# Kernel tuning notes

Hardware: AMD Instinct MI355X
Metric: run time of the kernel (lower is better)

Reference implementation:

```python
import jax, jax.numpy as jnp
import numpy as np

N = 50000       # nodes
E = 800000      # edges
F_IN = 128      # num_features
DIM = 64        # dim
D0 = 4 * DIM    # layer-0 width = 256
G = 256         # num graphs
EPS_BN = 1e-5


def _init_linear(key, fan_in, fan_out, bias=True):
    k1, k2 = jax.random.split(key)
    W = jax.random.normal(k1, (fan_in, fan_out), jnp.float32) * (1.0 / np.sqrt(fan_in))
    if bias:
        b = jax.random.normal(k2, (fan_out,), jnp.float32) * 0.01
        return W, b
    return W


def setup_inputs() -> dict:
    key = jax.random.key(0)
    ks = jax.random.split(key, 16)
    x = jax.random.normal(ks[0], (N, F_IN), jnp.float32)
    edge_index = jax.random.randint(ks[1], (2, E), 0, N, jnp.int32)
    edge_attr = jax.random.normal(ks[2], (E, 1), jnp.float32)
    batch = jnp.sort(jax.random.randint(ks[3], (N,), 0, G, jnp.int32))
    # conv0: in F_IN -> out D0, heads=1, edge_dim=1
    Wq0, bq0 = _init_linear(ks[4], F_IN, D0)
    Wk0, bk0 = _init_linear(ks[5], F_IN, D0)
    Wv0, bv0 = _init_linear(ks[6], F_IN, D0)
    We0 = _init_linear(ks[7], 1, D0, bias=False)   # lin_edge has no bias in PyG
    Ws0, bs0 = _init_linear(ks[8], F_IN, D0)       # lin_skip (root weight)
    # conv1: in D0 -> out DIM
    Wq1, bq1 = _init_linear(ks[9], D0, DIM)
    Wk1, bk1 = _init_linear(ks[10], D0, DIM)
    Wv1, bv1 = _init_linear(ks[11], D0, DIM)
    We1 = _init_linear(ks[12], 1, DIM, bias=False)
    Ws1, bs1 = _init_linear(ks[13], D0, DIM)
    # BatchNorm affine params
    gamma0 = jnp.ones((D0,), jnp.float32)
    beta0 = jnp.zeros((D0,), jnp.float32)
    gamma1 = jnp.ones((DIM,), jnp.float32)
    beta1 = jnp.zeros((DIM,), jnp.float32)
    return dict(x=x, edge_index=edge_index, edge_attr=edge_attr, batch=batch,
                Wq0=Wq0, bq0=bq0, Wk0=Wk0, bk0=bk0, Wv0=Wv0, bv0=bv0, We0=We0, Ws0=Ws0, bs0=bs0,
                gamma0=gamma0, beta0=beta0,
                Wq1=Wq1, bq1=bq1, Wk1=Wk1, bk1=bk1, Wv1=Wv1, bv1=bv1, We1=We1, Ws1=Ws1, bs1=bs1,
                gamma1=gamma1, beta1=beta1)


def _transformer_conv(x, edge_index, edge_attr, Wq, bq, Wk, bk, Wv, bv, We, Ws, bs):
    # PyG TransformerConv, heads=1, concat=True, root_weight=True, beta=False
    src, dst = edge_index[0], edge_index[1]
    n, d = x.shape[0], Wq.shape[1]
    q = x @ Wq + bq            # [N, d]
    k = x @ Wk + bk
    v = x @ Wv + bv
    e = edge_attr @ We          # [E, d]
    ke = k[src] + e             # key_j + edge embedding
    logits = jnp.sum(q[dst] * ke, axis=-1) / jnp.sqrt(jnp.asarray(d, jnp.float32))  # [E]
    # scatter-softmax over incoming edges of each dst node
    m = jax.ops.segment_max(logits, dst, num_segments=n)
    p = jnp.exp(logits - m[dst])
    s = jax.ops.segment_sum(p, dst, num_segments=n)
    alpha = p / (s[dst] + 1e-16)
    msg = (v[src] + e) * alpha[:, None]              # [E, d]
    out = jax.ops.segment_sum(msg, dst, num_segments=n)
    return out + x @ Ws + bs                          # root/skip connection


def _batch_norm(x, gamma, beta):
    mu = jnp.mean(x, axis=0)
    var = jnp.mean(jnp.square(x - mu), axis=0)  # biased var (torch training mode)
    return gamma * (x - mu) * jax.lax.rsqrt(var + EPS_BN) + beta


def _global_mean_pool(x, batch, num_graphs):
    s = jax.ops.segment_sum(x, batch, num_segments=num_graphs)
    c = jax.ops.segment_sum(jnp.ones((x.shape[0],), x.dtype), batch, num_segments=num_graphs)
    return s / jnp.maximum(c, 1.0)[:, None]


def reference(x, edge_index, edge_attr, batch,
              Wq0, bq0, Wk0, bk0, Wv0, bv0, We0, Ws0, bs0, gamma0, beta0,
              Wq1, bq1, Wk1, bk1, Wv1, bv1, We1, Ws1, bs1, gamma1, beta1):
    h0 = _batch_norm(_transformer_conv(x, edge_index, edge_attr,
                                       Wq0, bq0, Wk0, bk0, Wv0, bv0, We0, Ws0, bs0),
                     gamma0, beta0)                  # [N, D0]
    h1 = _batch_norm(_transformer_conv(h0, edge_index, edge_attr,
                                       Wq1, bq1, Wk1, bk1, Wv1, bv1, We1, Ws1, bs1),
                     gamma1, beta1)                  # [N, DIM]
    xpool = jnp.concatenate([_global_mean_pool(h0, batch, G),
                             _global_mean_pool(h1, batch, G)], axis=1)  # [G, D0+DIM]
    xs = jnp.concatenate([h0, h1], axis=1)                               # [N, D0+DIM]
    return (xpool, xs)
```

## Files before the change

kernel.cpp:

```cpp
#include <hip/hip_runtime.h>

constexpr int NN = 50000;
constexpr int NE = 800000;
constexpr int F_IN = 128;
constexpr int D0 = 256;
constexpr int D1 = 64;
constexpr int NG = 256;
constexpr float EPS_BN = 1e-5f;

typedef __attribute__((ext_vector_type(8))) short bf16x8;
typedef __attribute__((ext_vector_type(4))) float f32x4;
typedef __attribute__((ext_vector_type(8))) ushort u16x8;
typedef __attribute__((ext_vector_type(4))) ushort u16x4;

__device__ inline ushort f2bf(float f) {
    uint32_t u = __float_as_uint(f);
    uint32_t r = u + 0x7fff + ((u >> 16) & 1);
    return (ushort)(r >> 16);
}
__device__ inline float bf2f(ushort b) {
    return __uint_as_float((uint32_t)b << 16);
}

__global__ __launch_bounds__(256) void k_hist(const int* __restrict__ ei, int* __restrict__ cnt) {
    int e = blockIdx.x * 256 + threadIdx.x;
    if (e < NE) atomicAdd(&cnt[ei[NE + e]], 1);
}

__global__ __launch_bounds__(256) void k_scan1(const int* __restrict__ cnt,
                                               int* __restrict__ offs,
                                               int* __restrict__ bsum) {
    __shared__ int lds[256];
    int idx = blockIdx.x * 256 + threadIdx.x;
    int v = (idx < NN) ? cnt[idx] : 0;
    lds[threadIdx.x] = v;
    __syncthreads();
    #pragma unroll
    for (int off = 1; off < 256; off <<= 1) {
        int add = (threadIdx.x >= off) ? lds[threadIdx.x - off] : 0;
        __syncthreads();
        lds[threadIdx.x] += add;
        __syncthreads();
    }
    if (idx < NN) offs[idx] = lds[threadIdx.x] - v;
    if (threadIdx.x == 255) bsum[blockIdx.x] = lds[255];
}

__global__ __launch_bounds__(256) void k_scan2(const int* __restrict__ bsum,
                                               int* __restrict__ boff, int nblk) {
    __shared__ int lds[256];
    int v = (threadIdx.x < nblk) ? bsum[threadIdx.x] : 0;
    lds[threadIdx.x] = v;
    __syncthreads();
    #pragma unroll
    for (int off = 1; off < 256; off <<= 1) {
        int add = (threadIdx.x >= off) ? lds[threadIdx.x - off] : 0;
        __syncthreads();
        lds[threadIdx.x] += add;
        __syncthreads();
    }
    if (threadIdx.x < nblk) boff[threadIdx.x] = lds[threadIdx.x] - v;
}

__global__ __launch_bounds__(256) void k_scan3(int* __restrict__ offs,
                                               const int* __restrict__ boff,
                                               int* __restrict__ cursor) {
    int idx = blockIdx.x * 256 + threadIdx.x;
    if (idx < NN) {
        int o = offs[idx] + boff[blockIdx.x];
        offs[idx] = o;
        cursor[idx] = o;
    }
    if (idx == 0) offs[NN] = NE;
}

__global__ __launch_bounds__(256) void k_scatter(const int* __restrict__ ei,
                                                 const float* __restrict__ ea,
                                                 int* __restrict__ cursor,
                                                 int2* __restrict__ sedge) {
    int e = blockIdx.x * 256 + threadIdx.x;
    if (e < NE) {
        int d = ei[NE + e];
        int pos = atomicAdd(&cursor[d], 1);
        sedge[pos] = make_int2(ei[e], __float_as_int(ea[e]));
    }
}

__global__ __launch_bounds__(256) void k_f2bf4(const float* __restrict__ in,
                                               ushort* __restrict__ out, int n4) {
    for (int i = blockIdx.x * 256 + threadIdx.x; i < n4; i += gridDim.x * 256) {
        float4 v = *reinterpret_cast<const float4*>(&in[(size_t)i * 4]);
        ushort4 o;
        o.x = f2bf(v.x); o.y = f2bf(v.y); o.z = f2bf(v.z); o.w = f2bf(v.w);
        *reinterpret_cast<ushort4*>(&out[(size_t)i * 4]) = o;
    }
}

struct WPrep {
    const float* src[8];
    ushort* dst[8];
    int K[8];
    int D[8];
};
__global__ __launch_bounds__(256) void k_wprep(WPrep p) {
    int m = blockIdx.y;
    int K = p.K[m], D = p.D[m];
    int n = K * D;
    for (int idx = blockIdx.x * 256 + threadIdx.x; idx < n; idx += gridDim.x * 256) {
        int c = idx / K, k = idx - c * K;
        p.dst[m][idx] = f2bf(p.src[m][(size_t)k * D + c]);
    }
}

template<int K, int DOUT>
__global__ __launch_bounds__(256) void k_gemm_mfma(
    const ushort* __restrict__ Xb, const ushort* __restrict__ Wt,
    const float* __restrict__ B0, const float* __restrict__ B1,
    const float* __restrict__ B2, const float* __restrict__ B3,
    float* __restrict__ Oq, ushort* __restrict__ Ok,
    ushort* __restrict__ Ov, float* __restrict__ Oh)
{
    constexpr int BM = 128, BN = 64, BK = 32;
    __shared__ ushort Xs[BM][BK + 8];
    __shared__ ushort Wss[BN][BK + 8];

    int row0 = blockIdx.x * BM;
    int col0 = blockIdx.y * BN;
    int mat = col0 / DOUT;
    int mcol0 = col0 - mat * DOUT;
    const float* Bb = (mat == 0) ? B0 : (mat == 1) ? B1 : (mat == 2) ? B2 : B3;

    int t = threadIdx.x;
    int wid = t >> 6, lane = t & 63;
    int wr = wid >> 1, wc = wid & 1;
    int lr = lane & 15, lk = lane >> 4;

    f32x4 acc[4][2] = {};

    for (int k0 = 0; k0 < K; k0 += BK) {
        #pragma unroll
        for (int i = 0; i < 2; ++i) {
            int slot = t + i * 256;
            int r = slot >> 2, c8 = slot & 3;
            int gr = row0 + r;
            uint4 val = make_uint4(0, 0, 0, 0);
            if (gr < NN) val = *reinterpret_cast<const uint4*>(&Xb[(size_t)gr * K + k0 + c8 * 8]);
            *reinterpret_cast<uint4*>(&Xs[r][c8 * 8]) = val;
        }
        {
            int r = t >> 2, c8 = t & 3;
            uint4 val = *reinterpret_cast<const uint4*>(&Wt[(size_t)(col0 + r) * K + k0 + c8 * 8]);
            *reinterpret_cast<uint4*>(&Wss[r][c8 * 8]) = val;
        }
        __syncthreads();
        bf16x8 a[4], b[2];
        #pragma unroll
        for (int m = 0; m < 4; ++m)
            a[m] = *reinterpret_cast<const bf16x8*>(&Xs[wr * 64 + m * 16 + lr][lk * 8]);
        #pragma unroll
        for (int n = 0; n < 2; ++n)
            b[n] = *reinterpret_cast<const bf16x8*>(&Wss[wc * 32 + n * 16 + lr][lk * 8]);
        #pragma unroll
        for (int m = 0; m < 4; ++m)
            #pragma unroll
            for (int n = 0; n < 2; ++n)
                acc[m][n] = __builtin_amdgcn_mfma_f32_16x16x32_bf16(a[m], b[n], acc[m][n], 0, 0, 0);
        __syncthreads();
    }

    #pragma unroll
    for (int m = 0; m < 4; ++m) {
        #pragma unroll
        for (int n = 0; n < 2; ++n) {
            int gcol = mcol0 + wc * 32 + n * 16 + lr;
            float bias = Bb[gcol];
            #pragma unroll
            for (int r = 0; r < 4; ++r) {
                int grow = row0 + wr * 64 + m * 16 + lk * 4 + r;
                if (grow >= NN) continue;
                float vv = acc[m][n][r] + bias;
                size_t oidx = (size_t)grow * DOUT + gcol;
                if (mat == 0) Oq[oidx] = vv;
                else if (mat == 1) Ok[oidx] = f2bf(vv);
                else if (mat == 2) Ov[oidx] = f2bf(vv);
                else Oh[oidx] = vv;
            }
        }
    }
}

template<int D>
__global__ __launch_bounds__(256) void k_attn(
    const float* __restrict__ q, const ushort* __restrict__ kb, const ushort* __restrict__ vb,
    const float* __restrict__ We,
    const int2* __restrict__ sedge,
    const int* __restrict__ offs,
    float* __restrict__ hout)
{
    int wave = threadIdx.x >> 6;
    int lane = threadIdx.x & 63;
    int node = blockIdx.x * 4 + wave;
    if (node >= NN) return;
    int start = offs[node], stop = offs[node + 1];

    if constexpr (D == 256) {
        constexpr float scale = 0.0625f;
        int g = lane >> 5, sl = lane & 31;
        float q8[8], wel8[8];
        {
            float4 qa = *reinterpret_cast<const float4*>(&q[(size_t)node * 256 + sl * 8]);
            float4 qb = *reinterpret_cast<const float4*>(&q[(size_t)node * 256 + sl * 8 + 4]);
            q8[0] = qa.x; q8[1] = qa.y; q8[2] = qa.z; q8[3] = qa.w;
            q8[4] = qb.x; q8[5] = qb.y; q8[6] = qb.z; q8[7] = qb.w;
            float4 wa = *reinterpret_cast<const float4*>(&We[sl * 8]);
            float4 wb = *reinterpret_cast<const float4*>(&We[sl * 8 + 4]);
            wel8[0] = wa.x; wel8[1] = wa.y; wel8[2] = wa.z; wel8[3] = wa.w;
            wel8[4] = wb.x; wel8[5] = wb.y; wel8[6] = wb.z; wel8[7] = wb.w;
        }
        int deg = stop - start;
        int niter = (deg + 1) >> 1;
        float acc8[8] = {};
        float ssum = 0.f;

        int idx0 = start + g;
        bool val0 = idx0 < stop;
        int e0 = val0 ? idx0 : 0;
        int2 se0 = sedge[e0];
        u16x8 ku0 = *reinterpret_cast<const u16x8*>(&kb[(size_t)se0.x * 256 + sl * 8]);
        u16x8 vu0 = *reinterpret_cast<const u16x8*>(&vb[(size_t)se0.x * 256 + sl * 8]);

        for (int j = 0; j < niter; ++j) {
            int idx1 = start + 2 * (j + 1) + g;
            bool val1 = idx1 < stop;
            int e1 = val1 ? idx1 : 0;
            int2 se1 = sedge[e1];
            u16x8 ku1 = *reinterpret_cast<const u16x8*>(&kb[(size_t)se1.x * 256 + sl * 8]);
            u16x8 vu1 = *reinterpret_cast<const u16x8*>(&vb[(size_t)se1.x * 256 + sl * 8]);
            float eav = __int_as_float(se0.y);
            float ew[8];
            float dot = 0.f;
            #pragma unroll
            for (int c = 0; c < 8; ++c) {
                ew[c] = eav * wel8[c];
                dot = fmaf(q8[c], bf2f((ushort)ku0[c]) + ew[c], dot);
            }
            #pragma unroll
            for (int o = 1; o <= 16; o <<= 1) dot += __shfl_xor(dot, o);
            float p = val0 ? __expf(dot * scale) : 0.f;
            ssum += p;
            #pragma unroll
            for (int c = 0; c < 8; ++c)
                acc8[c] = fmaf(p, bf2f((ushort)vu0[c]) + ew[c], acc8[c]);
            val0 = val1; se0 = se1; ku0 = ku1; vu0 = vu1;
        }
        ssum += __shfl_xor(ssum, 32);
        #pragma unroll
        for (int c = 0; c < 8; ++c) acc8[c] += __shfl_xor(acc8[c], 32);
        float inv = 1.0f / (ssum + 1e-16f);
        float o4[4];
        #pragma unroll
        for (int c = 0; c < 4; ++c) o4[c] = g ? acc8[4 + c] : acc8[c];
        float* hp = &hout[(size_t)node * 256 + sl * 8 + g * 4];
        float4 cur = *reinterpret_cast<float4*>(hp);
        cur.x += o4[0] * inv; cur.y += o4[1] * inv;
        cur.z += o4[2] * inv; cur.w += o4[3] * inv;
        *reinterpret_cast<float4*>(hp) = cur;
    } else {
        constexpr float scale = 0.125f;
        int g = lane >> 4, sl = lane & 15;
        float q4[4], wel4[4];
        {
            float4 qa = *reinterpret_cast<const float4*>(&q[(size_t)node * 64 + sl * 4]);
            q4[0] = qa.x; q4[1] = qa.y; q4[2] = qa.z; q4[3] = qa.w;
            float4 wa = *reinterpret_cast<const float4*>(&We[sl * 4]);
            wel4[0] = wa.x; wel4[1] = wa.y; wel4[2] = wa.z; wel4[3] = wa.w;
        }
        int deg = stop - start;
        int niter = (deg + 3) >> 2;
        float acc4[4] = {};
        float ssum = 0.f;

        int idx0 = start + g;
        bool val0 = idx0 < stop;
        int e0 = val0 ? idx0 : 0;
        int2 se0 = sedge[e0];
        u16x4 ku0 = *reinterpret_cast<const u16x4*>(&kb[(size_t)se0.x * 64 + sl * 4]);
        u16x4 vu0 = *reinterpret_cast<const u16x4*>(&vb[(size_t)se0.x * 64 + sl * 4]);

        for (int j = 0; j < niter; ++j) {
            int idx1 = start + 4 * (j + 1) + g;
            bool val1 = idx1 < stop;
            int e1 = val1 ? idx1 : 0;
            int2 se1 = sedge[e1];
            u16x4 ku1 = *reinterpret_cast<const u16x4*>(&kb[(size_t)se1.x * 64 + sl * 4]);
            u16x4 vu1 = *reinterpret_cast<const u16x4*>(&vb[(size_t)se1.x * 64 + sl * 4]);
            float eav = __int_as_float(se0.y);
            float ew[4];
            float dot = 0.f;
            #pragma unroll
            for (int c = 0; c < 4; ++c) {
                ew[c] = eav * wel4[c];
                dot = fmaf(q4[c], bf2f((ushort)ku0[c]) + ew[c], dot);
            }
            #pragma unroll
            for (int o = 1; o <= 8; o <<= 1) dot += __shfl_xor(dot, o);
            float p = val0 ? __expf(dot * scale) : 0.f;
            ssum += p;
            #pragma unroll
            for (int c = 0; c < 4; ++c)
                acc4[c] = fmaf(p, bf2f((ushort)vu0[c]) + ew[c], acc4[c]);
            val0 = val1; se0 = se1; ku0 = ku1; vu0 = vu1;
        }
        ssum += __shfl_xor(ssum, 16);
        ssum += __shfl_xor(ssum, 32);
        #pragma unroll
        for (int c = 0; c < 4; ++c) {
            acc4[c] += __shfl_xor(acc4[c], 16);
            acc4[c] += __shfl_xor(acc4[c], 32);
        }
        float inv = 1.0f / (ssum + 1e-16f);
        float av = acc4[0];
        av = (g == 1) ? acc4[1] : av;
        av = (g == 2) ? acc4[2] : av;
        av = (g == 3) ? acc4[3] : av;
        hout[(size_t)node * 64 + sl * 4 + g] += av * inv;
    }
}

template<int D>
__global__ __launch_bounds__(256) void k_bnstats(const float* __restrict__ h,
                                                 float* __restrict__ sums,
                                                 int rows_per_block) {
    constexpr int NSUB = 256 / D;
    int col = threadIdx.x % D;
    int sub = threadIdx.x / D;
    int r0 = blockIdx.x * rows_per_block;
    int r1 = min(r0 + rows_per_block, NN);
    float s = 0.f, ss = 0.f;
    for (int r = r0 + sub; r < r1; r += NSUB) {
        float x = h[(size_t)r * D + col];
        s += x; ss += x * x;
    }
    atomicAdd(&sums[col], s);
    atomicAdd(&sums[D + col], ss);
}

template<int D>
__global__ void k_bnfin(const float* __restrict__ sums,
                        const float* __restrict__ gamma, const float* __restrict__ beta,
                        float* __restrict__ ab) {
    int c = threadIdx.x;
    if (c >= D) return;
    float mean = sums[c] / (float)NN;
    float var = sums[D + c] / (float)NN - mean * mean;
    float a = gamma[c] * rsqrtf(var + EPS_BN);
    ab[c] = a;
    ab[D + c] = beta[c] - mean * a;
}

__global__ __launch_bounds__(256) void k_bnapply0(float* __restrict__ h,
                                                  const float* __restrict__ ab,
                                                  float* __restrict__ xs,
                                                  ushort* __restrict__ h0b) {
    int idx = blockIdx.x * 256 + threadIdx.x;
    int n = idx >> 6, c4 = idx & 63;
    float4 x4 = *reinterpret_cast<float4*>(&h[(size_t)idx * 4]);
    float4 a4 = *reinterpret_cast<const float4*>(&ab[c4 * 4]);
    float4 b4 = *reinterpret_cast<const float4*>(&ab[256 + c4 * 4]);
    float4 r;
    r.x = a4.x * x4.x + b4.x; r.y = a4.y * x4.y + b4.y;
    r.z = a4.z * x4.z + b4.z; r.w = a4.w * x4.w + b4.w;
    *reinterpret_cast<float4*>(&xs[(size_t)n * 320 + c4 * 4]) = r;
    ushort4 o;
    o.x = f2bf(r.x); o.y = f2bf(r.y); o.z = f2bf(r.z); o.w = f2bf(r.w);
    *reinterpret_cast<ushort4*>(&h0b[(size_t)idx * 4]) = o;
}

__global__ __launch_bounds__(256) void k_bnapply1(const float* __restrict__ h,
                                                  const float* __restrict__ ab,
                                                  float* __restrict__ xs) {
    int idx = blockIdx.x * 256 + threadIdx.x;
    int n = idx >> 4, c4 = idx & 15;
    float4 x4 = *reinterpret_cast<const float4*>(&h[(size_t)idx * 4]);
    float4 a4 = *reinterpret_cast<const float4*>(&ab[c4 * 4]);
    float4 b4 = *reinterpret_cast<const float4*>(&ab[64 + c4 * 4]);
    float4 r;
    r.x = a4.x * x4.x + b4.x; r.y = a4.y * x4.y + b4.y;
    r.z = a4.z * x4.z + b4.z; r.w = a4.w * x4.w + b4.w;
    *reinterpret_cast<float4*>(&xs[(size_t)n * 320 + 256 + c4 * 4]) = r;
}

__global__ __launch_bounds__(256) void k_pool(const float* __restrict__ xs,
                                              const int* __restrict__ batch,
                                              float* __restrict__ xpool) {
    int g = blockIdx.x;
    __shared__ int se[2];
    if (threadIdx.x < 2) {
        int target = g + threadIdx.x;
        int lo = 0, hi = NN;
        while (lo < hi) {
            int mid = (lo + hi) >> 1;
            if (batch[mid] < target) lo = mid + 1; else hi = mid;
        }
        se[threadIdx.x] = lo;
    }
    __syncthreads();
    int start = se[0], stop = se[1];
    float cnt = fmaxf((float)(stop - start), 1.0f);
    for (int c = threadIdx.x; c < 320; c += 256) {
        float s = 0.f;
        for (int r = start; r < stop; ++r) s += xs[(size_t)r * 320 + c];
        xpool[(size_t)g * 320 + c] = s / cnt;
    }
}

extern "C" void kernel_launch(void* const* d_in, const int* in_sizes, int n_in,
                              void* d_out, int out_size, void* d_ws, size_t ws_size,
                              hipStream_t stream) {
    const float* x     = (const float*)d_in[0];
    const int*   ei    = (const int*)d_in[1];
    const float* ea    = (const float*)d_in[2];
    const int*   batch = (const int*)d_in[3];
    const float *Wq0 = (const float*)d_in[4],  *bq0 = (const float*)d_in[5];
    const float *Wk0 = (const float*)d_in[6],  *bk0 = (const float*)d_in[7];
    const float *Wv0 = (const float*)d_in[8],  *bv0 = (const float*)d_in[9];
    const float *We0 = (const float*)d_in[10];
    const float *Ws0 = (const float*)d_in[11], *bs0 = (const float*)d_in[12];
    const float *gamma0 = (const float*)d_in[13], *beta0 = (const float*)d_in[14];
    const float *Wq1 = (const float*)d_in[15], *bq1 = (const float*)d_in[16];
    const float *Wk1 = (const float*)d_in[17], *bk1 = (const float*)d_in[18];
    const float *Wv1 = (const float*)d_in[19], *bv1 = (const float*)d_in[20];
    const float *We1 = (const float*)d_in[21];
    const float *Ws1 = (const float*)d_in[22], *bs1 = (const float*)d_in[23];
    const float *gamma1 = (const float*)d_in[24], *beta1 = (const float*)d_in[25];

    char* ws = (char*)d_ws;
    size_t off = 0;
    auto alloc = [&](size_t bytes) -> char* {
        char* p = ws + off;
        off += (bytes + 255) & ~(size_t)255;
        return p;
    };
    float*  q0   = (float*)alloc((size_t)NN * D0 * 4);
    ushort* k0b  = (ushort*)alloc((size_t)NN * D0 * 2);
    ushort* v0b  = (ushort*)alloc((size_t)NN * D0 * 2);
    float*  h0   = (float*)alloc((size_t)NN * D0 * 4);
    ushort* xbuf = (ushort*)alloc((size_t)NN * D0 * 2);
    int2*  sedge = (int2*)alloc((size_t)NE * 8);
    int*   cnt    = (int*)alloc((size_t)(NN + 1) * 4);
    int*   offs   = (int*)alloc((size_t)(NN + 1) * 4);
    int*   cursor = (int*)alloc((size_t)(NN + 1) * 4);
    int*   bsum   = (int*)alloc(256 * 4);
    int*   boff   = (int*)alloc(256 * 4);
    float* sums0  = (float*)alloc(2 * D0 * 4);
    float* ab0    = (float*)alloc(2 * D0 * 4);
    float* sums1  = (float*)alloc(2 * D1 * 4);
    float* ab1    = (float*)alloc(2 * D1 * 4);
    ushort* wt0   = (ushort*)alloc((size_t)4 * D0 * F_IN * 2);
    ushort* wt1   = (ushort*)alloc((size_t)4 * D1 * D0 * 2);

    ushort* xb  = xbuf;
    ushort* h0b = xbuf;

    float*  q1  = q0;
    ushort* k1b = (ushort*)(q0 + (size_t)NN * D1);
    ushort* v1b = k1b + (size_t)NN * D1;
    float*  h1  = (float*)(v1b + (size_t)NN * D1);

    float* xpool = (float*)d_out;
    float* xs = (float*)d_out + (size_t)NG * 320;

    const int NBLK = (NN + 255) / 256;
    const int BN_BLK = (NN + 63) / 64;

    hipMemsetAsync(cnt, 0, (NN + 1) * 4, stream);
    k_hist<<<(NE + 255) / 256, 256, 0, stream>>>(ei, cnt);
    k_scan1<<<NBLK, 256, 0, stream>>>(cnt, offs, bsum);
    k_scan2<<<1, 256, 0, stream>>>(bsum, boff, NBLK);
    k_scan3<<<NBLK, 256, 0, stream>>>(offs, boff, cursor);
    k_scatter<<<(NE + 255) / 256, 256, 0, stream>>>(ei, ea, cursor, sedge);

    k_f2bf4<<<2048, 256, 0, stream>>>(x, xb, NN * F_IN / 4);
    WPrep wp;
    wp.src[0] = Wq0; wp.src[1] = Wk0; wp.src[2] = Wv0; wp.src[3] = Ws0;
    wp.src[4] = Wq1; wp.src[5] = Wk1; wp.src[6] = Wv1; wp.src[7] = Ws1;
    for (int m = 0; m < 4; ++m) { wp.K[m] = F_IN; wp.D[m] = D0; wp.dst[m] = wt0 + (size_t)m * D0 * F_IN; }
    for (int m = 0; m < 4; ++m) { wp.K[4+m] = D0; wp.D[4+m] = D1; wp.dst[4+m] = wt1 + (size_t)m * D1 * D0; }
    k_wprep<<<dim3(64, 8), 256, 0, stream>>>(wp);

    k_gemm_mfma<F_IN, D0><<<dim3((NN + 127) / 128, 16), 256, 0, stream>>>(
        xb, wt0, bq0, bk0, bv0, bs0, q0, k0b, v0b, h0);
    k_attn<D0><<<(NN + 3) / 4, 256, 0, stream>>>(q0, k0b, v0b, We0, sedge, offs, h0);
    hipMemsetAsync(sums0, 0, 2 * D0 * 4, stream);
    k_bnstats<D0><<<BN_BLK, 256, 0, stream>>>(h0, sums0, 64);
    k_bnfin<D0><<<1, D0, 0, stream>>>(sums0, gamma0, beta0, ab0);
    k_bnapply0<<<(NN * 64 + 255) / 256, 256, 0, stream>>>(h0, ab0, xs, h0b);

    k_gemm_mfma<D0, D1><<<dim3((NN + 127) / 128, 4), 256, 0, stream>>>(
        h0b, wt1, bq1, bk1, bv1, bs1, q1, k1b, v1b, h1);
    k_attn<D1><<<(NN + 3) / 4, 256, 0, stream>>>(q1, k1b, v1b, We1, sedge, offs, h1);
    hipMemsetAsync(sums1, 0, 2 * D1 * 4, stream);
    k_bnstats<D1><<<BN_BLK, 256, 0, stream>>>(h1, sums1, 64);
    k_bnfin<D1><<<1, D1, 0, stream>>>(sums1, gamma1, beta1, ab1);
    k_bnapply1<<<(NN * 16 + 255) / 256, 256, 0, stream>>>(h1, ab1, xs);

    k_pool<<<NG, 256, 0, stream>>>(xs, batch, xpool);
}
```

Measured before the change: 765.2 us.

## Interleave K/V rows, factor edge term out of attention loop, deepen prefetch

K and V are stored interleaved per node, so each gathered source row brings both into one contiguous span and uses one address computation. The edge-attribute term is factored algebraically: q·We is precomputed once, the per-edge score adds eav*qWe, and the value-side edge contribution is accumulated as a scalar sum and applied once after the loop. The gather prefetch depth goes from one iteration ahead to two, which adds registers and may lower occupancy. Layer-1 buffers now alias layer-0 buffers (kv1 on kv0, h1 on h0), relying on stream ordering.

After: 768.6 us. About the same (+0.4%).

```diff
diff --git a/kernel.cpp b/kernel.cpp
--- a/kernel.cpp
+++ b/kernel.cpp
@@ -117,8 +117,8 @@
     const ushort* __restrict__ Xb, const ushort* __restrict__ Wt,
     const float* __restrict__ B0, const float* __restrict__ B1,
     const float* __restrict__ B2, const float* __restrict__ B3,
-    float* __restrict__ Oq, ushort* __restrict__ Ok,
-    ushort* __restrict__ Ov, float* __restrict__ Oh)
+    float* __restrict__ Oq, ushort* __restrict__ Okv,
+    float* __restrict__ Oh)
 {
     constexpr int BM = 128, BN = 64, BK = 32;
     __shared__ ushort Xs[BM][BK + 8];
@@ -179,11 +179,10 @@
                 int grow = row0 + wr * 64 + m * 16 + lk * 4 + r;
                 if (grow >= NN) continue;
                 float vv = acc[m][n][r] + bias;
-                size_t oidx = (size_t)grow * DOUT + gcol;
-                if (mat == 0) Oq[oidx] = vv;
-                else if (mat == 1) Ok[oidx] = f2bf(vv);
-                else if (mat == 2) Ov[oidx] = f2bf(vv);
-                else Oh[oidx] = vv;
+                if (mat == 0) Oq[(size_t)grow * DOUT + gcol] = vv;
+                else if (mat == 1) Okv[(size_t)grow * (2 * DOUT) + gcol] = f2bf(vv);
+                else if (mat == 2) Okv[(size_t)grow * (2 * DOUT) + DOUT + gcol] = f2bf(vv);
+                else Oh[(size_t)grow * DOUT + gcol] = vv;
             }
         }
     }
@@ -191,7 +190,7 @@
 
 template<int D>
 __global__ __launch_bounds__(256) void k_attn(
-    const float* __restrict__ q, const ushort* __restrict__ kb, const ushort* __restrict__ vb,
+    const float* __restrict__ q, const ushort* __restrict__ kvb,
     const float* __restrict__ We,
     const int2* __restrict__ sedge,
     const int* __restrict__ offs,
@@ -217,42 +216,49 @@
             wel8[0] = wa.x; wel8[1] = wa.y; wel8[2] = wa.z; wel8[3] = wa.w;
             wel8[4] = wb.x; wel8[5] = wb.y; wel8[6] = wb.z; wel8[7] = wb.w;
         }
-        int deg = stop - start;
-        int niter = (deg + 1) >> 1;
+        float qWe = 0.f;
+        #pragma unroll
+        for (int c = 0; c < 8; ++c) qWe = fmaf(q8[c], wel8[c], qWe);
+        #pragma unroll
+        for (int o = 1; o <= 16; o <<= 1) qWe += __shfl_xor(qWe, o);
+
+        int niter = (stop - start + 1) >> 1;
         float acc8[8] = {};
-        float ssum = 0.f;
-
-        int idx0 = start + g;
-        bool val0 = idx0 < stop;
-        int e0 = val0 ? idx0 : 0;
-        int2 se0 = sedge[e0];
-        u16x8 ku0 = *reinterpret_cast<const u16x8*>(&kb[(size_t)se0.x * 256 + sl * 8]);
-        u16x8 vu0 = *reinterpret_cast<const u16x8*>(&vb[(size_t)se0.x * 256 + sl * 8]);
+        float ssum = 0.f, sse = 0.f;
+
+        bool val0, val1; int2 se0, se1;
+        u16x8 ku0, vu0, ku1, vu1;
+        auto LOAD = [&](int j, bool& val, int2& se, u16x8& ku, u16x8& vu) {
+            int idx = start + 2 * j + g;
+            val = idx < stop;
+            int e = val ? idx : 0;
+            se = sedge[e];
+            const ushort* base = &kvb[(size_t)se.x * 512 + sl * 8];
+            ku = *reinterpret_cast<const u16x8*>(base);
+            vu = *reinterpret_cast<const u16x8*>(base + 256);
+        };
+        LOAD(0, val0, se0, ku0, vu0);
+        LOAD(1, val1, se1, ku1, vu1);
 
         for (int j = 0; j < niter; ++j) {
-            int idx1 = start + 2 * (j + 1) + g;
-            bool val1 = idx1 < stop;
-            int e1 = val1 ? idx1 : 0;
-            int2 se1 = sedge[e1];
-            u16x8 ku1 = *reinterpret_cast<const u16x8*>(&kb[(size_t)se1.x * 256 + sl * 8]);
-            u16x8 vu1 = *reinterpret_cast<const u16x8*>(&vb[(size_t)se1.x * 256 + sl * 8]);
+            bool val2; int2 se2; u16x8 ku2, vu2;
+            LOAD(j + 2, val2, se2, ku2, vu2);
+            float dot = 0.f;
+            #pragma unroll
+            for (int c = 0; c < 8; ++c) dot = fmaf(q8[c], bf2f((ushort)ku0[c]), dot);
+            #pragma unroll
+            for (int o = 1; o <= 16; o <<= 1) dot += __shfl_xor(dot, o);
             float eav = __int_as_float(se0.y);
-            float ew[8];
-            float dot = 0.f;
-            #pragma unroll
-            for (int c = 0; c < 8; ++c) {
-                ew[c] = eav * wel8[c];
-                dot = fmaf(q8[c], bf2f((ushort)ku0[c]) + ew[c], dot);
-            }
-            #pragma unroll
-            for (int o = 1; o <= 16; o <<= 1) dot += __shfl_xor(dot, o);
-            float p = val0 ? __expf(dot * scale) : 0.f;
+            float p = val0 ? __expf((dot + eav * qWe) * scale) : 0.f;
             ssum += p;
-            #pragma unroll
-            for (int c = 0; c < 8; ++c)
-                acc8[c] = fmaf(p, bf2f((ushort)vu0[c]) + ew[c], acc8[c]);
+            sse = fmaf(p, eav, sse);
+            #pragma unroll
+            for (int c = 0; c < 8; ++c) acc8[c] = fmaf(p, bf2f((ushort)vu0[c]), acc8[c]);
             val0 = val1; se0 = se1; ku0 = ku1; vu0 = vu1;
-        }
+            val1 = val2; se1 = se2; ku1 = ku2; vu1 = vu2;
+        }
+        #pragma unroll
+        for (int c = 0; c < 8; ++c) acc8[c] = fmaf(sse, wel8[c], acc8[c]);
         ssum += __shfl_xor(ssum, 32);
         #pragma unroll
         for (int c = 0; c < 8; ++c) acc8[c] += __shfl_xor(acc8[c], 32);
@@ -275,42 +281,49 @@
             float4 wa = *reinterpret_cast<const float4*>(&We[sl * 4]);
             wel4[0] = wa.x; wel4[1] = wa.y; wel4[2] = wa.z; wel4[3] = wa.w;
         }
-        int deg = stop - start;
-        int niter = (deg + 3) >> 2;
+        float qWe = 0.f;
+        #pragma unroll
+        for (int c = 0; c < 4; ++c) qWe = fmaf(q4[c], wel4[c], qWe);
+        #pragma unroll
+        for (int o = 1; o <= 8; o <<= 1) qWe += __shfl_xor(qWe, o);
+
+        int niter = (stop - start + 3) >> 2;
         float acc4[4] = {};
-        float ssum = 0.f;
-
-        int idx0 = start + g;
-        bool val0 = idx0 < stop;
-        int e0 = val0 ? idx0 : 0;
-        int2 se0 = sedge[e0];
-        u16x4 ku0 = *reinterpret_cast<const u16x4*>(&kb[(size_t)se0.x * 64 + sl * 4]);
-        u16x4 vu0 = *reinterpret_cast<const u16x4*>(&vb[(size_t)se0.x * 64 + sl * 4]);
+        float ssum = 0.f, sse = 0.f;
+
+        bool val0, val1; int2 se0, se1;
+        u16x4 ku0, vu0, ku1, vu1;
+        auto LOAD = [&](int j, bool& val, int2& se, u16x4& ku, u16x4& vu) {
+            int idx = start + 4 * j + g;
+            val = idx < stop;
+            int e = val ? idx : 0;
+            se = sedge[e];
+            const ushort* base = &kvb[(size_t)se.x * 128 + sl * 4];
+            ku = *reinterpret_cast<const u16x4*>(base);
+            vu = *reinterpret_cast<const u16x4*>(base + 64);
+        };
+        LOAD(0, val0, se0, ku0, vu0);
+        LOAD(1, val1, se1, ku1, vu1);
 
         for (int j = 0; j < niter; ++j) {
-            int idx1 = start + 4 * (j + 1) + g;
-            bool val1 = idx1 < stop;
-            int e1 = val1 ? idx1 : 0;
-            int2 se1 = sedge[e1];
-            u16x4 ku1 = *reinterpret_cast<const u16x4*>(&kb[(size_t)se1.x * 64 + sl * 4]);
-            u16x4 vu1 = *reinterpret_cast<const u16x4*>(&vb[(size_t)se1.x * 64 + sl * 4]);
+            bool val2; int2 se2; u16x4 ku2, vu2;
+            LOAD(j + 2, val2, se2, ku2, vu2);
+            float dot = 0.f;
+            #pragma unroll
+            for (int c = 0; c < 4; ++c) dot = fmaf(q4[c], bf2f((ushort)ku0[c]), dot);
+            #pragma unroll
+            for (int o = 1; o <= 8; o <<= 1) dot += __shfl_xor(dot, o);
             float eav = __int_as_float(se0.y);
-            float ew[4];
-            float dot = 0.f;
-            #pragma unroll
-            for (int c = 0; c < 4; ++c) {
-                ew[c] = eav * wel4[c];
-                dot = fmaf(q4[c], bf2f((ushort)ku0[c]) + ew[c], dot);
-            }
-            #pragma unroll
-            for (int o = 1; o <= 8; o <<= 1) dot += __shfl_xor(dot, o);
-            float p = val0 ? __expf(dot * scale) : 0.f;
+            float p = val0 ? __expf((dot + eav * qWe) * scale) : 0.f;
             ssum += p;
-            #pragma unroll
-            for (int c = 0; c < 4; ++c)
-                acc4[c] = fmaf(p, bf2f((ushort)vu0[c]) + ew[c], acc4[c]);
+            sse = fmaf(p, eav, sse);
+            #pragma unroll
+            for (int c = 0; c < 4; ++c) acc4[c] = fmaf(p, bf2f((ushort)vu0[c]), acc4[c]);
             val0 = val1; se0 = se1; ku0 = ku1; vu0 = vu1;
-        }
+            val1 = val2; se1 = se2; ku1 = ku2; vu1 = vu2;
+        }
+        #pragma unroll
+        for (int c = 0; c < 4; ++c) acc4[c] = fmaf(sse, wel4[c], acc4[c]);
         ssum += __shfl_xor(ssum, 16);
         ssum += __shfl_xor(ssum, 32);
         #pragma unroll
@@ -442,8 +455,7 @@
         return p;
     };
     float*  q0   = (float*)alloc((size_t)NN * D0 * 4);
-    ushort* k0b  = (ushort*)alloc((size_t)NN * D0 * 2);
-    ushort* v0b  = (ushort*)alloc((size_t)NN * D0 * 2);
+    ushort* kv0  = (ushort*)alloc((size_t)NN * 2 * D0 * 2);
     float*  h0   = (float*)alloc((size_t)NN * D0 * 4);
     ushort* xbuf = (ushort*)alloc((size_t)NN * D0 * 2);
     int2*  sedge = (int2*)alloc((size_t)NE * 8);
@@ -463,9 +475,8 @@
     ushort* h0b = xbuf;
 
     float*  q1  = q0;
-    ushort* k1b = (ushort*)(q0 + (size_t)NN * D1);
-    ushort* v1b = k1b + (size_t)NN * D1;
-    float*  h1  = (float*)(v1b + (size_t)NN * D1);
+    ushort* kv1 = kv0;
+    float*  h1  = h0;
 
     float* xpool = (float*)d_out;
     float* xs = (float*)d_out + (size_t)NG * 320;
@@ -489,16 +500,16 @@
     k_wprep<<<dim3(64, 8), 256, 0, stream>>>(wp);
 
     k_gemm_mfma<F_IN, D0><<<dim3((NN + 127) / 128, 16), 256, 0, stream>>>(
-        xb, wt0, bq0, bk0, bv0, bs0, q0, k0b, v0b, h0);
-    k_attn<D0><<<(NN + 3) / 4, 256, 0, stream>>>(q0, k0b, v0b, We0, sedge, offs, h0);
+        xb, wt0, bq0, bk0, bv0, bs0, q0, kv0, h0);
+    k_attn<D0><<<(NN + 3) / 4, 256, 0, stream>>>(q0, kv0, We0, sedge, offs, h0);
     hipMemsetAsync(sums0, 0, 2 * D0 * 4, stream);
     k_bnstats<D0><<<BN_BLK, 256, 0, stream>>>(h0, sums0, 64);
     k_bnfin<D0><<<1, D0, 0, stream>>>(sums0, gamma0, beta0, ab0);
     k_bnapply0<<<(NN * 64 + 255) / 256, 256, 0, stream>>>(h0, ab0, xs, h0b);
 
     k_gemm_mfma<D0, D1><<<dim3((NN + 127) / 128, 4), 256, 0, stream>>>(
-        h0b, wt1, bq1, bk1, bv1, bs1, q1, k1b, v1b, h1);
-    k_attn<D1><<<(NN + 3) / 4, 256, 0, stream>>>(q1, k1b, v1b, We1, sedge, offs, h1);
+        h0b, wt1, bq1, bk1, bv1, bs1, q1, kv1, h1);
+    k_attn<D1><<<(NN + 3) / 4, 256, 0, stream>>>(q1, kv1, We1, sedge, offs, h1);
     hipMemsetAsync(sums1, 0, 2 * D1 * 4, stream);
     k_bnstats<D1><<<BN_BLK, 256, 0, stream>>>(h1, sums1, 64);
     k_bnfin<D1><<<1, D1, 0, stream>>>(sums1, gamma1, beta1, ab1);
```
